# Kernel tuning notes

Measured on AMD Instinct MI355X. Metric: run time of the kernel, lower is better.

## Reference

```python
import jax, jax.numpy as jnp
import numpy as np

N_SAMPLE = 256
POS_IOU_THRESH = 0.7
NEG_IOU_THRESH = 0.3
POS_RATIO = 0.5


def _bbox_iou(bbox_a, bbox_b):
    # bbox_a: [K,4], bbox_b: [G,4] in (x1,y1,x2,y2)
    tl = jnp.maximum(bbox_a[:, None, :2], bbox_b[None, :, :2])  # [K,G,2]
    br = jnp.minimum(bbox_a[:, None, 2:], bbox_b[None, :, 2:])  # [K,G,2]
    wh = br - tl
    inter = wh[..., 0] * wh[..., 1] * jnp.all(tl < br, axis=2)  # [K,G]
    area_a = (bbox_a[:, 2] - bbox_a[:, 0]) * (bbox_a[:, 3] - bbox_a[:, 1])
    area_b = (bbox_b[:, 2] - bbox_b[:, 0]) * (bbox_b[:, 3] - bbox_b[:, 1])
    return inter / (area_a[:, None] + area_b[None, :] - inter)


def _bbox2loc(src_bbox, dst_bbox):
    eps = jnp.asarray(np.finfo(np.float32).eps, src_bbox.dtype)
    width = jnp.maximum(src_bbox[:, 2] - src_bbox[:, 0], eps)
    height = jnp.maximum(src_bbox[:, 3] - src_bbox[:, 1], eps)
    ctr_x = src_bbox[:, 0] + 0.5 * (src_bbox[:, 2] - src_bbox[:, 0])
    ctr_y = src_bbox[:, 1] + 0.5 * (src_bbox[:, 3] - src_bbox[:, 1])
    base_w = dst_bbox[:, 2] - dst_bbox[:, 0]
    base_h = dst_bbox[:, 3] - dst_bbox[:, 1]
    base_cx = dst_bbox[:, 0] + 0.5 * base_w
    base_cy = dst_bbox[:, 1] + 0.5 * base_h
    dx = (base_cx - ctr_x) / width
    dy = (base_cy - ctr_y) / height
    dw = jnp.log(base_w / width)
    dh = jnp.log(base_h / height)
    return jnp.stack([dx, dy, dw, dh], axis=1)  # [K,4]


def _masked_rank(mask, priority):
    # rank (0-based, by priority) of each element within the masked subset;
    # elements outside the mask get ranks >= subset size.
    key = jnp.where(mask, priority, jnp.inf)
    order = jnp.argsort(key)
    n = order.shape[0]
    return jnp.zeros((n,), jnp.int32).at[order].set(jnp.arange(n, dtype=jnp.int32))


def _make_boxes(key, n, coord_max, wh_min, wh_max):
    k1, k2 = jax.random.split(key)
    xy = jax.random.uniform(k1, (n, 2), jnp.float32, 0.0, coord_max)
    wh = jax.random.uniform(k2, (n, 2), jnp.float32, wh_min, wh_max)
    return jnp.concatenate([xy, xy + wh], axis=1)  # valid x1<x2, y1<y2


def setup_inputs() -> dict:
    key = jax.random.key(0)
    ka, kb = jax.random.split(key)
    anchor = _make_boxes(ka, 131072, 800.0, 8.0, 256.0)
    bbox = _make_boxes(kb, 256, 800.0, 16.0, 300.0)
    return {"anchor": anchor, "bbox": bbox}


def reference(anchor, bbox):
    K = anchor.shape[0]
    G = bbox.shape[0]
    ious = _bbox_iou(anchor, bbox)  # [K,G]
    argmax_ious = jnp.argmax(ious, axis=1).astype(jnp.int32)  # best gt per anchor
    max_ious = jnp.max(ious, axis=1)
    gt_argmax_ious = jnp.argmax(ious, axis=0)  # best anchor per gt, [G]
    # force each gt's best anchor to be assigned to that gt
    argmax_ious = argmax_ious.at[gt_argmax_ious].set(jnp.arange(G, dtype=jnp.int32))

    label = jnp.full((K,), -1, jnp.int32)
    label = jnp.where(max_ious < NEG_IOU_THRESH, 0, label)
    label = jnp.where(max_ious >= POS_IOU_THRESH, 1, label)
    label = label.at[gt_argmax_ious].set(1)

    # random subsampling of positives / negatives (fixed key, jit-friendly)
    skey = jax.random.key(42)
    k1, k2 = jax.random.split(skey)
    p_pos = jax.random.uniform(k1, (K,))
    p_neg = jax.random.uniform(k2, (K,))

    n_pos = int(POS_RATIO * N_SAMPLE)
    pos_mask = label == 1
    pos_rank = _masked_rank(pos_mask, p_pos)
    label = jnp.where(pos_mask & (pos_rank >= n_pos), -1, label)

    n_neg = N_SAMPLE - jnp.sum(label == 1)
    neg_mask = label == 0
    neg_rank = _masked_rank(neg_mask, p_neg)
    label = jnp.where(neg_mask & (neg_rank >= n_neg), -1, label)

    loc = _bbox2loc(anchor, bbox[argmax_ious])  # [K,4]
    has_pos = jnp.any(label > 0)
    loc = jnp.where(has_pos, loc, jnp.zeros_like(loc))
    return loc, label
```

## Files before the change

### kernel.cpp

```cpp
#include <hip/hip_runtime.h>
#include <stdint.h>

#define K_ANCH 131072
#define G_BOX  256
#define NPOS_TGT 128
#define NSAMPLE 256
#define POS_CAP 8192
#define NEG_CAP 32768
#define NPART 16

struct TF2 { uint32_t a, b; };

__host__ __device__ constexpr uint32_t rotl32(uint32_t v, int d) {
  return (v << d) | (v >> (32 - d));
}

__host__ __device__ constexpr TF2 threefry(uint32_t k0, uint32_t k1,
                                           uint32_t x0, uint32_t x1) {
  const uint32_t ks0 = k0, ks1 = k1, ks2 = k0 ^ k1 ^ 0x1BD11BDAu;
  const int R0[4] = {13, 15, 26, 6};
  const int R1[4] = {17, 29, 16, 24};
  x0 += ks0; x1 += ks1;
  for (int r = 0; r < 4; ++r) { x0 += x1; x1 = rotl32(x1, R0[r]); x1 ^= x0; }
  x0 += ks1; x1 += ks2 + 1u;
  for (int r = 0; r < 4; ++r) { x0 += x1; x1 = rotl32(x1, R1[r]); x1 ^= x0; }
  x0 += ks2; x1 += ks0 + 2u;
  for (int r = 0; r < 4; ++r) { x0 += x1; x1 = rotl32(x1, R0[r]); x1 ^= x0; }
  x0 += ks0; x1 += ks1 + 3u;
  for (int r = 0; r < 4; ++r) { x0 += x1; x1 = rotl32(x1, R1[r]); x1 ^= x0; }
  x0 += ks1; x1 += ks2 + 4u;
  for (int r = 0; r < 4; ++r) { x0 += x1; x1 = rotl32(x1, R0[r]); x1 ^= x0; }
  x0 += ks2; x1 += ks0 + 5u;
  return TF2{x0, x1};
}

constexpr TF2 KPOS = threefry(0u, 42u, 0u, 0u);
constexpr TF2 KNEG = threefry(0u, 42u, 0u, 1u);

__device__ __forceinline__ uint32_t rbits(TF2 k, uint32_t i) {
  TF2 r = threefry(k.a, k.b, 0u, i);
  return r.a ^ r.b;
}

__device__ __forceinline__ float p_from_bits(uint32_t bits) {
  uint32_t fb = 0x3f800000u | (bits >> 9);
  float f = __uint_as_float(fb) - 1.0f;
  return fmaxf(f, 0.0f);
}

__device__ __forceinline__ uint64_t prio_key(float p, uint32_t idx) {
  return ((uint64_t)__float_as_uint(p) << 32) | (uint64_t)idx;
}

__device__ __forceinline__ uint32_t iou_bits(float4 a, float area_a, float4 b, float ab) {
  #pragma clang fp contract(off)
  float tlx = fmaxf(a.x, b.x), tly = fmaxf(a.y, b.y);
  float brx = fminf(a.z, b.z), bry = fminf(a.w, b.w);
  float w = brx - tlx, h = bry - tly;
  float wh = w * h;
  bool ok = (tlx < brx) && (tly < bry);
  float inter = ok ? wh : 0.0f;
  float u = (area_a + ab) - inter;
  float v = inter / u;
  return __float_as_uint(v);
}

struct ScalarBlk {
  unsigned long long cutoff[2];
  int B_pos, r_pos, B_neg, r_neg;
  int do_pos, do_neg, pos_kept, pad;
};

__global__ __launch_bounds__(256) void k_fused(const float4* __restrict__ anchor,
                                               const float4* __restrict__ bbox,
                                               int* __restrict__ argmax,
                                               int* __restrict__ label,
                                               unsigned long long* __restrict__ gkey_part) {
  __shared__ float4 gts[G_BOX];
  __shared__ float gab[G_BOX];
  __shared__ uint32_t ioum[128 * 65];
  __shared__ uint32_t xb[4][64];
  __shared__ int xi[4][64];
  int tid = threadIdx.x;
  int al = tid & 63, q = tid >> 6;
  int abase = blockIdx.x * 64;
  int i = abase + al;

  float4 bbv = bbox[tid];
  gts[tid] = bbv;
  {
    #pragma clang fp contract(off)
    gab[tid] = (bbv.z - bbv.x) * (bbv.w - bbv.y);
  }
  __syncthreads();

  float4 a = anchor[i];
  float area_a;
  {
    #pragma clang fp contract(off)
    area_a = (a.z - a.x) * (a.w - a.y);
  }
  uint32_t bestbits = 0u; int bidx = 0;

  #pragma unroll
  for (int h = 0; h < 2; ++h) {
    int hg = h * 128;
    #pragma unroll 8
    for (int s = 0; s < 32; ++s) {
      int c = q * 32 + s;
      int g = hg + c;
      float4 b = gts[g];
      float ab = gab[g];
      uint32_t vb = iou_bits(a, area_a, b, ab);
      if (vb > bestbits) { bestbits = vb; bidx = g; }
      ioum[c * 65 + al] = vb;
    }
    __syncthreads();
    if (tid < 128) {
      int c = tid;
      uint32_t cb = ioum[c * 65 + 0]; int ca = 0;
      #pragma unroll 8
      for (int aa = 1; aa < 64; ++aa) {
        uint32_t v = ioum[c * 65 + aa];
        if (v > cb) { cb = v; ca = aa; }
      }
      unsigned long long key =
          ((unsigned long long)cb << 32) |
          (unsigned long long)(~(uint32_t)(abase + ca));
      atomicMax(&gkey_part[(blockIdx.x & (NPART - 1)) * G_BOX + hg + c], key);
    }
    __syncthreads();
  }

  xb[q][al] = bestbits; xi[q][al] = bidx;
  __syncthreads();
  if (tid < 64) {
    uint32_t bestb = xb[0][tid]; int bi = xi[0][tid];
    #pragma unroll
    for (int qq = 1; qq < 4; ++qq) {
      uint32_t ob = xb[qq][tid]; int og = xi[qq][tid];
      if (ob > bestb || (ob == bestb && og < bi)) { bestb = ob; bi = og; }
    }
    argmax[i] = bi;
    float best = __uint_as_float(bestb);
    int lbl = -1;
    if (best < 0.3f) lbl = 0;
    if (best >= 0.7f) lbl = 1;
    label[i] = lbl;
  }
}

__global__ void k_force(const unsigned long long* __restrict__ gkey_part,
                        int* __restrict__ argmax, int* __restrict__ label) {
  __shared__ int ga[G_BOX];
  int tid = threadIdx.x;
  unsigned long long best = gkey_part[tid];
  #pragma unroll
  for (int p = 1; p < NPART; ++p) {
    unsigned long long o = gkey_part[p * G_BOX + tid];
    if (o > best) best = o;
  }
  ga[tid] = (int)(~(uint32_t)(best & 0xffffffffull));
  __syncthreads();
  label[ga[tid]] = 1;
  if (tid == 0) {
    for (int t = 0; t < G_BOX; ++t) argmax[ga[t]] = t;
  }
}

__global__ __launch_bounds__(256) void k_hist(const int* __restrict__ label,
                                              uint32_t* __restrict__ hist) {
  int i = blockIdx.x * 256 + threadIdx.x;
  int lbl = label[i];
  if (lbl < 0) return;
  TF2 k = (lbl == 1) ? KPOS : KNEG;
  float p = p_from_bits(rbits(k, (uint32_t)i));
  int b = (int)(p * 1024.0f); if (b > 1023) b = 1023;
  atomicAdd((unsigned int*)&hist[(lbl == 1 ? 0 : 1024) + b], 1u);
}

__global__ __launch_bounds__(256) void k_select(const uint32_t* __restrict__ hist,
                                                ScalarBlk* __restrict__ sc) {
  __shared__ uint32_t h[2048];
  for (int t = threadIdx.x; t < 2048; t += 256) h[t] = hist[t];
  __syncthreads();
  if (threadIdx.x != 0) return;
  uint32_t total_pos = 0, total_neg = 0;
  for (int b = 0; b < 1024; ++b) total_pos += h[b];
  for (int b = 0; b < 1024; ++b) total_neg += h[1024 + b];
  int pos_kept = total_pos < (uint32_t)NPOS_TGT ? (int)total_pos : NPOS_TGT;
  int n_neg = NSAMPLE - pos_kept;
  sc->pos_kept = pos_kept;
  if (total_pos <= (uint32_t)NPOS_TGT) {
    sc->do_pos = 0; sc->cutoff[0] = ~0ull;
  } else {
    uint32_t cum = 0; int B = 0;
    for (; B < 1024; ++B) { if (cum + h[B] > (uint32_t)NPOS_TGT) break; cum += h[B]; }
    sc->do_pos = 1; sc->B_pos = B; sc->r_pos = NPOS_TGT - (int)cum;
  }
  if (total_neg <= (uint32_t)n_neg) {
    sc->do_neg = 0; sc->cutoff[1] = ~0ull;
  } else {
    uint32_t cum = 0; int B = 0;
    for (; B < 1024; ++B) { if (cum + h[1024 + B] > (uint32_t)n_neg) break; cum += h[1024 + B]; }
    sc->do_neg = 1; sc->B_neg = B; sc->r_neg = n_neg - (int)cum;
  }
}

__global__ __launch_bounds__(256) void k_collect(const int* __restrict__ label,
                                                 uint64_t* __restrict__ pos_list,
                                                 uint64_t* __restrict__ neg_list,
                                                 uint32_t* __restrict__ counters,
                                                 const ScalarBlk* __restrict__ sc) {
  int i = blockIdx.x * 256 + threadIdx.x;
  int lbl = label[i];
  if (lbl < 0) return;
  if (lbl == 1) {
    if (!sc->do_pos) return;
    float p = p_from_bits(rbits(KPOS, (uint32_t)i));
    int b = (int)(p * 1024.0f); if (b > 1023) b = 1023;
    if (b != sc->B_pos) return;
    uint32_t slot = atomicAdd((unsigned int*)&counters[0], 1u);
    if (slot < POS_CAP) pos_list[slot] = prio_key(p, (uint32_t)i);
  } else {
    if (!sc->do_neg) return;
    float p = p_from_bits(rbits(KNEG, (uint32_t)i));
    int b = (int)(p * 1024.0f); if (b > 1023) b = 1023;
    if (b != sc->B_neg) return;
    uint32_t slot = atomicAdd((unsigned int*)&counters[1], 1u);
    if (slot < NEG_CAP) neg_list[slot] = prio_key(p, (uint32_t)i);
  }
}

__global__ __launch_bounds__(256) void k_cutoff(const uint64_t* __restrict__ pos_list,
                                                const uint64_t* __restrict__ neg_list,
                                                const uint32_t* __restrict__ counters,
                                                ScalarBlk* __restrict__ sc) {
  int cls = blockIdx.x;
  int doit = (cls == 0) ? sc->do_pos : sc->do_neg;
  if (!doit) return;
  const uint64_t* list = (cls == 0) ? pos_list : neg_list;
  int cap = (cls == 0) ? POS_CAP : NEG_CAP;
  int m = (int)counters[cls]; if (m > cap) m = cap;
  int r = (cls == 0) ? sc->r_pos : sc->r_neg;
  for (int j = threadIdx.x; j < m; j += 256) {
    uint64_t kj = list[j];
    int rank = 0;
    for (int t = 0; t < m; ++t) rank += (list[t] < kj) ? 1 : 0;
    if (rank == r) sc->cutoff[cls] = (unsigned long long)kj;
  }
}

__global__ __launch_bounds__(256) void k_final(const float4* __restrict__ anchor,
                                               const float4* __restrict__ bbox,
                                               const int* __restrict__ argmax,
                                               const int* __restrict__ label,
                                               const ScalarBlk* __restrict__ sc,
                                               float* __restrict__ out) {
  #pragma clang fp contract(off)
  int i = blockIdx.x * 256 + threadIdx.x;
  int lbl = label[i];
  if (lbl == 1) {
    float p = p_from_bits(rbits(KPOS, (uint32_t)i));
    if (prio_key(p, (uint32_t)i) >= sc->cutoff[0]) lbl = -1;
  } else if (lbl == 0) {
    float p = p_from_bits(rbits(KNEG, (uint32_t)i));
    if (prio_key(p, (uint32_t)i) >= sc->cutoff[1]) lbl = -1;
  }
  out[K_ANCH * 4 + i] = (float)lbl;

  float4 a = anchor[i];
  float4 b = bbox[argmax[i]];
  const float eps = 1.1920928955078125e-07f;
  float w  = fmaxf(a.z - a.x, eps);
  float h  = fmaxf(a.w - a.y, eps);
  float cx = a.x + 0.5f * (a.z - a.x);
  float cy = a.y + 0.5f * (a.w - a.y);
  float bw = b.z - b.x, bh = b.w - b.y;
  float bcx = b.x + 0.5f * bw, bcy = b.y + 0.5f * bh;
  float dx = (bcx - cx) / w, dy = (bcy - cy) / h;
  float dw = logf(bw / w), dh = logf(bh / h);
  float4 o;
  if (sc->pos_kept > 0) o = make_float4(dx, dy, dw, dh);
  else o = make_float4(0.f, 0.f, 0.f, 0.f);
  ((float4*)out)[i] = o;
}

extern "C" void kernel_launch(void* const* d_in, const int* in_sizes, int n_in,
                              void* d_out, int out_size, void* d_ws, size_t ws_size,
                              hipStream_t stream) {
  const float4* anchor = (const float4*)d_in[0];
  const float4* bbox   = (const float4*)d_in[1];
  char* ws = (char*)d_ws;

  uint32_t* hist     = (uint32_t*)(ws);
  uint32_t* counters = (uint32_t*)(ws + 8192);
  unsigned long long* gkey_part = (unsigned long long*)(ws + 16384);
  ScalarBlk* sc      = (ScalarBlk*)(ws + 49152);
  int* argmax        = (int*)(ws + 65536);
  int* label         = (int*)(ws + 65536 + 524288);
  uint64_t* pos_list = (uint64_t*)(ws + 65536 + 1048576);
  uint64_t* neg_list = pos_list + POS_CAP;

  (void)hipMemsetAsync(ws, 0, 49152, stream);
  k_fused  <<<2048, 256, 0, stream>>>(anchor, bbox, argmax, label, gkey_part);
  k_force  <<<1,    256, 0, stream>>>(gkey_part, argmax, label);
  k_hist   <<<512,  256, 0, stream>>>(label, hist);
  k_select <<<1,    256, 0, stream>>>(hist, sc);
  k_collect<<<512,  256, 0, stream>>>(label, pos_list, neg_list, counters, sc);
  k_cutoff <<<2,    256, 0, stream>>>(pos_list, neg_list, counters, sc);
  k_final  <<<512,  256, 0, stream>>>(anchor, bbox, argmax, label, sc, (float*)d_out);
}
```

Baseline: 129.7 us.

## Split per-gt column argmax into 64-wide tiles reduced by all threads

The IoU tile is now processed in four rounds of 64 ground-truth boxes instead of two rounds of 128. Each column reduction over the block's 64 anchors is first done by all 256 threads, each scanning 16 anchors, and then 64 threads combine the four partial results. Before, 128 threads each scanned 64 anchors serially. The change also halves the shared-memory tile, which may allow more resident blocks. The cost is more barriers per block and an extra partial-result buffer.

```diff
diff --git a/kernel.cpp b/kernel.cpp
--- a/kernel.cpp
+++ b/kernel.cpp
@@ -78,7 +78,9 @@
                                                unsigned long long* __restrict__ gkey_part) {
   __shared__ float4 gts[G_BOX];
   __shared__ float gab[G_BOX];
-  __shared__ uint32_t ioum[128 * 65];
+  __shared__ uint32_t tile[64 * 65];
+  __shared__ uint32_t pb[4 * 64];
+  __shared__ int pi_[4 * 64];
   __shared__ uint32_t xb[4][64];
   __shared__ int xi[4][64];
   int tid = threadIdx.x;
@@ -102,36 +104,47 @@
   }
   uint32_t bestbits = 0u; int bidx = 0;
 
+  int col2 = tid & 63, seg = tid >> 6;
   #pragma unroll
-  for (int h = 0; h < 2; ++h) {
-    int hg = h * 128;
-    #pragma unroll 8
-    for (int s = 0; s < 32; ++s) {
-      int c = q * 32 + s;
-      int g = hg + c;
+  for (int r = 0; r < 4; ++r) {
+    int rbase = r * 64;
+    #pragma unroll
+    for (int s = 0; s < 16; ++s) {
+      int c = q * 16 + s;
+      int g = rbase + c;
       float4 b = gts[g];
       float ab = gab[g];
       uint32_t vb = iou_bits(a, area_a, b, ab);
       if (vb > bestbits) { bestbits = vb; bidx = g; }
-      ioum[c * 65 + al] = vb;
+      tile[c * 65 + al] = vb;
     }
     __syncthreads();
-    if (tid < 128) {
-      int c = tid;
-      uint32_t cb = ioum[c * 65 + 0]; int ca = 0;
-      #pragma unroll 8
-      for (int aa = 1; aa < 64; ++aa) {
-        uint32_t v = ioum[c * 65 + aa];
-        if (v > cb) { cb = v; ca = aa; }
+    {
+      int a0 = seg * 16;
+      uint32_t cb = tile[col2 * 65 + a0]; int ca = a0;
+      #pragma unroll
+      for (int aa = 1; aa < 16; ++aa) {
+        uint32_t v = tile[col2 * 65 + a0 + aa];
+        if (v > cb) { cb = v; ca = a0 + aa; }
+      }
+      pb[seg * 64 + col2] = cb; pi_[seg * 64 + col2] = ca;
+    }
+    __syncthreads();
+    if (tid < 64) {
+      uint32_t cb = pb[tid]; int ca = pi_[tid];
+      #pragma unroll
+      for (int sg = 1; sg < 4; ++sg) {
+        uint32_t v = pb[sg * 64 + tid];
+        if (v > cb) { cb = v; ca = pi_[sg * 64 + tid]; }
       }
       unsigned long long key =
           ((unsigned long long)cb << 32) |
           (unsigned long long)(~(uint32_t)(abase + ca));
-      atomicMax(&gkey_part[(blockIdx.x & (NPART - 1)) * G_BOX + hg + c], key);
+      atomicMax(&gkey_part[(blockIdx.x & (NPART - 1)) * G_BOX + rbase + tid], key);
     }
-    __syncthreads();
-  }
-
+  }
+
+  __syncthreads();
   xb[q][al] = bestbits; xi[q][al] = bidx;
   __syncthreads();
   if (tid < 64) {
```

Measured after the change: 136.0 us. 1.05x slower.
